# Kernel optimization log

Measured on AMD Instinct MI355X. Metric: run time of the kernel, lower is better.

The kernel has to match this reference:

```python
import jax, jax.numpy as jnp
import numpy as np

N = 50000        # num_nodes
E = 500000       # num_edges (avg degree 16)
EMB = 32         # node embedding dim
EDGE_DIM = 385   # EMBEDDING_DIM(384) + 1 grade
OC = 16          # out_channels
NEG_SLOPE = 0.2


def _gatv2(x, src, dst, eattr, Wl, bl, Wr, br, We, att, bias, heads, out_ch, n, concat):
    # lin_l -> source (x_j), lin_r -> target (x_i); PyG edge_index[0]=src, [1]=dst
    xl = (x @ Wl + bl).reshape(-1, heads, out_ch)   # [N,H,C]
    xr = (x @ Wr + br).reshape(-1, heads, out_ch)   # [N,H,C]
    ea = (eattr @ We).reshape(-1, heads, out_ch)    # [E,H,C]
    xj = xl[src]                                    # [E,H,C] gathered source
    xi = xr[dst]                                    # [E,H,C] gathered target
    e = jax.nn.leaky_relu(xj + xi + ea, NEG_SLOPE)
    logits = jnp.einsum('ehc,hc->eh', e, att)       # [E,H]
    # segment softmax over edges sharing the same target node
    m = jax.ops.segment_max(logits, dst, num_segments=n)
    m = jnp.where(jnp.isfinite(m), m, 0.0)
    ex = jnp.exp(logits - m[dst])
    s = jax.ops.segment_sum(ex, dst, num_segments=n)
    alpha = ex / (s[dst] + 1e-16)                   # [E,H]
    out = jax.ops.segment_sum(xj * alpha[..., None], dst, num_segments=n)  # [N,H,C]
    if concat:
        out = out.reshape(n, heads * out_ch)
    else:
        out = out.mean(axis=1)
    return out + bias


def setup_inputs() -> dict:
    key = jax.random.key(0)
    ks = jax.random.split(key, 32)
    f = lambda k, s, sc=0.1: (jax.random.normal(k, s, dtype=jnp.float32) * sc)
    inp = {}
    inp['node_ids'] = jnp.arange(N, dtype=jnp.int32)
    inp['edge_index'] = jax.random.randint(ks[0], (2, E), 0, N, dtype=jnp.int32)
    inp['edge_attr'] = f(ks[1], (E, EDGE_DIM))
    inp['node_emb'] = f(ks[2], (N, EMB))
    # layer 1: in=32, heads=4, out=16, concat -> 64
    inp['l1_Wl'] = f(ks[3], (EMB, 4 * OC)); inp['l1_bl'] = jnp.zeros((4 * OC,), jnp.float32)
    inp['l1_Wr'] = f(ks[4], (EMB, 4 * OC)); inp['l1_br'] = jnp.zeros((4 * OC,), jnp.float32)
    inp['l1_We'] = f(ks[5], (EDGE_DIM, 4 * OC))
    inp['l1_att'] = f(ks[6], (4, OC)); inp['l1_bias'] = jnp.zeros((4 * OC,), jnp.float32)
    # layer 2: in=64, heads=2, out=16, concat -> 32
    inp['l2_Wl'] = f(ks[7], (4 * OC, 2 * OC)); inp['l2_bl'] = jnp.zeros((2 * OC,), jnp.float32)
    inp['l2_Wr'] = f(ks[8], (4 * OC, 2 * OC)); inp['l2_br'] = jnp.zeros((2 * OC,), jnp.float32)
    inp['l2_We'] = f(ks[9], (EDGE_DIM, 2 * OC))
    inp['l2_att'] = f(ks[10], (2, OC)); inp['l2_bias'] = jnp.zeros((2 * OC,), jnp.float32)
    # layer 3: in=32, heads=1, out=16, mean -> 16
    inp['l3_Wl'] = f(ks[11], (2 * OC, OC)); inp['l3_bl'] = jnp.zeros((OC,), jnp.float32)
    inp['l3_Wr'] = f(ks[12], (2 * OC, OC)); inp['l3_br'] = jnp.zeros((OC,), jnp.float32)
    inp['l3_We'] = f(ks[13], (EDGE_DIM, OC))
    inp['l3_att'] = f(ks[14], (1, OC)); inp['l3_bias'] = jnp.zeros((OC,), jnp.float32)
    # edge MLP: 2*16 -> 64 -> 32 -> 1
    inp['mlp_W1'] = f(ks[15], (2 * OC, 64)); inp['mlp_b1'] = jnp.zeros((64,), jnp.float32)
    inp['mlp_W2'] = f(ks[16], (64, 32)); inp['mlp_b2'] = jnp.zeros((32,), jnp.float32)
    inp['mlp_W3'] = f(ks[17], (32, 1)); inp['mlp_b3'] = jnp.zeros((1,), jnp.float32)
    return inp


def reference(node_ids, edge_index, edge_attr, node_emb,
              l1_Wl, l1_bl, l1_Wr, l1_br, l1_We, l1_att, l1_bias,
              l2_Wl, l2_bl, l2_Wr, l2_br, l2_We, l2_att, l2_bias,
              l3_Wl, l3_bl, l3_Wr, l3_br, l3_We, l3_att, l3_bias,
              mlp_W1, mlp_b1, mlp_W2, mlp_b2, mlp_W3, mlp_b3):
    src, dst = edge_index[0], edge_index[1]
    x = node_emb[node_ids]                                   # [N,32]
    x1 = jax.nn.elu(_gatv2(x, src, dst, edge_attr, l1_Wl, l1_bl, l1_Wr, l1_br,
                           l1_We, l1_att, l1_bias, 4, OC, N, True))
    x2 = jax.nn.elu(_gatv2(x1, src, dst, edge_attr, l2_Wl, l2_bl, l2_Wr, l2_br,
                           l2_We, l2_att, l2_bias, 2, OC, N, True))
    x3 = _gatv2(x2, src, dst, edge_attr, l3_Wl, l3_bl, l3_Wr, l3_br,
                l3_We, l3_att, l3_bias, 1, OC, N, False)     # [N,16]
    h = jnp.concatenate([x3[src], x3[dst]], axis=1)          # [E,32]
    h = jax.nn.relu(h @ mlp_W1 + mlp_b1)
    h = jax.nn.relu(h @ mlp_W2 + mlp_b2)
    return (h @ mlp_W3 + mlp_b3).squeeze(-1)                 # [E]
```

## Files before the change

### kernel.cpp

```cpp
#include <hip/hip_runtime.h>

#define DEVINL __device__ __forceinline__

DEVINL unsigned fenc(float f) {
    unsigned u = __float_as_uint(f);
    return (u & 0x80000000u) ? ~u : (u | 0x80000000u);
}
DEVINL float fdec(unsigned k) {
    unsigned u = (k & 0x80000000u) ? (k ^ 0x80000000u) : ~k;
    return __uint_as_float(u);
}

DEVINL void gload_lds4(const float* g, float* l) {
    __builtin_amdgcn_global_load_lds(
        (const __attribute__((address_space(1))) unsigned int*)(const void*)g,
        (__attribute__((address_space(3))) unsigned int*)(void*)l,
        4, 0, 0);
}

__global__ void zero_kernel(float* __restrict__ p, long n) {
    long i = (long)blockIdx.x * blockDim.x + threadIdx.x;
    long stride = (long)gridDim.x * blockDim.x;
    for (; i < n; i += stride) p[i] = 0.f;
}

template<int IN, int HC>
__global__ __launch_bounds__(256) void node_transform(
    const float* __restrict__ x, const int* __restrict__ gather,
    const float* __restrict__ Wl, const float* __restrict__ bl,
    const float* __restrict__ Wr, const float* __restrict__ br,
    float* __restrict__ xl, float* __restrict__ xr, int N)
{
    __shared__ float Wls[IN * HC];
    __shared__ float Wrs[IN * HC];
    for (int i = threadIdx.x; i < IN * HC; i += 256) { Wls[i] = Wl[i]; Wrs[i] = Wr[i]; }
    __syncthreads();
    constexpr int NPB = 256 / HC;
    const int c = threadIdx.x % HC;
    const int n = blockIdx.x * NPB + threadIdx.x / HC;
    if (n >= N) return;
    const int row = gather ? gather[n] : n;
    const float* xp = x + (long)row * IN;
    float al = bl[c], ar = br[c];
#pragma unroll
    for (int k = 0; k < IN; ++k) {
        float v = xp[k];
        al = fmaf(v, Wls[k * HC + c], al);
        ar = fmaf(v, Wrs[k * HC + c], ar);
    }
    xl[(long)n * HC + c] = al;
    xr[(long)n * HC + c] = ar;
}

template<int HC, int OPT, int EPT>
__global__ __launch_bounds__(256) void gat_edge(
    const float* __restrict__ eattr,
    const float* __restrict__ xl, const float* __restrict__ xr,
    const float* __restrict__ We, const float* __restrict__ att,
    const int* __restrict__ src, const int* __restrict__ dst,
    float* __restrict__ logits, unsigned* __restrict__ mkey, int E)
{
    constexpr int H = HC / 16;
    constexpr int TX = HC / OPT;
    constexpr int TY = 256 / TX;
    constexpr int TILE_E = TY * EPT;
    constexpr int KC = 32;
    constexpr int NKM = 12;
    static_assert(TILE_E == 128, "tile geometry");
    static_assert((KC * HC) % 256 == 0, "B staging");
    static_assert((TILE_E * KC) / 256 == 16, "A staging");

    __shared__ float As[TILE_E * KC];
    __shared__ float Bs[KC * HC];
    __shared__ float Blast[HC];
    __shared__ float part[TILE_E][TX + 1];

    const int tid = threadIdx.x;
    const int tx = tid % TX, ty = tid / TX;
    const long eblk = (long)blockIdx.x * TILE_E;

    if (tid < HC) Blast[tid] = We[384 * HC + tid];

    float acc[EPT][OPT];
#pragma unroll
    for (int i = 0; i < EPT; ++i)
#pragma unroll
        for (int j = 0; j < OPT; ++j) acc[i][j] = 0.f;

    for (int kc = 0; kc < NKM; ++kc) {
        const int k0 = kc * KC;
#pragma unroll
        for (int i = 0; i < 16; ++i) {
            const int idx = tid + i * 256;
            const int row = idx >> 5;
            const int c   = idx & 31;
            const int klog = (((c >> 2) ^ ((row >> 2) & 7)) << 2) | (c & 3);
            long ge = eblk + row;
            ge = (ge < E) ? ge : (long)(E - 1);
            gload_lds4(eattr + ge * 385 + (k0 + klog), &As[idx]);
        }
        constexpr int BELEM = KC * HC / 256;
#pragma unroll
        for (int i = 0; i < BELEM; ++i) {
            const int idx = tid + i * 256;
            gload_lds4(We + (long)k0 * HC + idx, &Bs[idx]);
        }
        asm volatile("s_waitcnt vmcnt(0)" ::: "memory");
        __syncthreads();

#pragma unroll
        for (int g = 0; g < 8; ++g) {
            float a[EPT][4];
#pragma unroll
            for (int i = 0; i < EPT; ++i) {
                const int row = ty * EPT + i;
                const float4 v = *(const float4*)&As[row * KC + ((g ^ ((row >> 2) & 7)) << 2)];
                a[i][0] = v.x; a[i][1] = v.y; a[i][2] = v.z; a[i][3] = v.w;
            }
#pragma unroll
            for (int q = 0; q < 4; ++q) {
                float b[OPT];
#pragma unroll
                for (int j = 0; j < OPT; j += 4) {
                    const float4 bv = *(const float4*)&Bs[(g * 4 + q) * HC + tx * OPT + j];
                    b[j] = bv.x; b[j + 1] = bv.y; b[j + 2] = bv.z; b[j + 3] = bv.w;
                }
#pragma unroll
                for (int i = 0; i < EPT; ++i)
#pragma unroll
                    for (int j = 0; j < OPT; ++j)
                        acc[i][j] = fmaf(a[i][q], b[j], acc[i][j]);
            }
        }
        __syncthreads();
    }

    const int h = (tx * OPT) / 16;
    const int cb = (tx * OPT) % 16;
    float av[OPT], bl[OPT];
#pragma unroll
    for (int j = 0; j < OPT; ++j) {
        av[j] = att[h * 16 + cb + j];
        bl[j] = Blast[tx * OPT + j];
    }

#pragma unroll
    for (int i = 0; i < EPT; ++i) {
        const int el = ty * EPT + i;
        const long ge = eblk + el;
        float p = 0.f;
        if (ge < E) {
            const float a384 = eattr[ge * 385 + 384];
            const float* xlp = xl + (long)src[ge] * HC + tx * OPT;
            const float* xrp = xr + (long)dst[ge] * HC + tx * OPT;
#pragma unroll
            for (int j = 0; j < OPT; j += 4) {
                const float4 vj = *(const float4*)(xlp + j);
                const float4 vi = *(const float4*)(xrp + j);
                float t0 = fmaf(a384, bl[j + 0], acc[i][j + 0]) + vj.x + vi.x;
                float t1 = fmaf(a384, bl[j + 1], acc[i][j + 1]) + vj.y + vi.y;
                float t2 = fmaf(a384, bl[j + 2], acc[i][j + 2]) + vj.z + vi.z;
                float t3 = fmaf(a384, bl[j + 3], acc[i][j + 3]) + vj.w + vi.w;
                t0 = (t0 > 0.f) ? t0 : 0.2f * t0;
                t1 = (t1 > 0.f) ? t1 : 0.2f * t1;
                t2 = (t2 > 0.f) ? t2 : 0.2f * t2;
                t3 = (t3 > 0.f) ? t3 : 0.2f * t3;
                p = fmaf(t0, av[j + 0], p);
                p = fmaf(t1, av[j + 1], p);
                p = fmaf(t2, av[j + 2], p);
                p = fmaf(t3, av[j + 3], p);
            }
        }
        part[el][tx] = p;
    }
    __syncthreads();

    constexpr int G = 16 / OPT;
    for (int idx = tid; idx < TILE_E * H; idx += 256) {
        const int e = idx / H, hh = idx % H;
        const long ge = eblk + e;
        if (ge < E) {
            float l = 0.f;
#pragma unroll
            for (int g = 0; g < G; ++g) l += part[e][hh * G + g];
            logits[ge * H + hh] = l;
            atomicMax(&mkey[(unsigned)dst[ge] * H + hh], fenc(l));
        }
    }
}

template<int H>
__global__ __launch_bounds__(256) void softmax_ex(
    float* __restrict__ lg, const unsigned* __restrict__ mkey,
    float* __restrict__ ssum, const int* __restrict__ dst, int E)
{
    int idx = blockIdx.x * 256 + threadIdx.x;
    if (idx >= E * H) return;
    int e = idx / H, h = idx % H;
    int d = dst[e];
    float m = fdec(mkey[d * H + h]);
    float ex = expf(lg[idx] - m);
    lg[idx] = ex;
    atomicAdd(&ssum[d * H + h], ex);
}

template<int HC>
__global__ __launch_bounds__(256) void aggregate(
    const float* __restrict__ ex, const float* __restrict__ ssum,
    const float* __restrict__ xl, const int* __restrict__ src,
    const int* __restrict__ dst, float* __restrict__ acc, int E)
{
    constexpr int H = HC / 16;
    long idx = (long)blockIdx.x * 256 + threadIdx.x;
    if (idx >= (long)E * HC) return;
    int e = (int)(idx / HC), c = (int)(idx % HC);
    int h = c / 16;
    int d = dst[e];
    float alpha = ex[(long)e * H + h] / (ssum[d * H + h] + 1e-16f);
    atomicAdd(&acc[(long)d * HC + c], xl[(long)src[e] * HC + c] * alpha);
}

__global__ __launch_bounds__(256) void finalize_k(
    const float* __restrict__ acc, const float* __restrict__ bias,
    float* __restrict__ xout, int total, int HC, int do_elu)
{
    int idx = blockIdx.x * 256 + threadIdx.x;
    if (idx >= total) return;
    float v = acc[idx] + bias[idx % HC];
    if (do_elu) v = (v > 0.f) ? v : expm1f(v);
    xout[idx] = v;
}

__global__ __launch_bounds__(256) void edge_mlp(
    const float* __restrict__ x3, const int* __restrict__ src, const int* __restrict__ dst,
    const float* __restrict__ W1, const float* __restrict__ b1,
    const float* __restrict__ W2, const float* __restrict__ b2,
    const float* __restrict__ W3, const float* __restrict__ b3,
    float* __restrict__ out, int E)
{
    int e = blockIdx.x * 256 + threadIdx.x;
    if (e >= E) return;
    float in[32];
    const float* xs = x3 + (long)src[e] * 16;
    const float* xd = x3 + (long)dst[e] * 16;
#pragma unroll
    for (int k = 0; k < 16; k += 4) {
        float4 a = *(const float4*)(xs + k);
        float4 b = *(const float4*)(xd + k);
        in[k] = a.x; in[k + 1] = a.y; in[k + 2] = a.z; in[k + 3] = a.w;
        in[16 + k] = b.x; in[16 + k + 1] = b.y; in[16 + k + 2] = b.z; in[16 + k + 3] = b.w;
    }
    float h1[64];
#pragma unroll
    for (int j = 0; j < 64; ++j) h1[j] = b1[j];
#pragma unroll
    for (int k = 0; k < 32; ++k) {
        float a = in[k];
#pragma unroll
        for (int j = 0; j < 64; ++j) h1[j] = fmaf(a, W1[k * 64 + j], h1[j]);
    }
    float h2[32];
#pragma unroll
    for (int j = 0; j < 32; ++j) h2[j] = b2[j];
#pragma unroll
    for (int k = 0; k < 64; ++k) {
        float a = h1[k] > 0.f ? h1[k] : 0.f;
#pragma unroll
        for (int j = 0; j < 32; ++j) h2[j] = fmaf(a, W2[k * 32 + j], h2[j]);
    }
    float o = b3[0];
#pragma unroll
    for (int j = 0; j < 32; ++j) {
        float a = h2[j] > 0.f ? h2[j] : 0.f;
        o = fmaf(a, W3[j], o);
    }
    out[e] = o;
}

extern "C" void kernel_launch(void* const* d_in, const int* in_sizes, int n_in,
                              void* d_out, int out_size, void* d_ws, size_t ws_size,
                              hipStream_t stream) {
    const int N = in_sizes[0];
    const int E = in_sizes[1] / 2;

    const int*   node_ids = (const int*)d_in[0];
    const int*   src      = (const int*)d_in[1];
    const int*   dst      = src + E;
    const float* eattr    = (const float*)d_in[2];
    const float* node_emb = (const float*)d_in[3];
    const float* l1_Wl = (const float*)d_in[4],  *l1_bl = (const float*)d_in[5];
    const float* l1_Wr = (const float*)d_in[6],  *l1_br = (const float*)d_in[7];
    const float* l1_We = (const float*)d_in[8],  *l1_att = (const float*)d_in[9];
    const float* l1_bias = (const float*)d_in[10];
    const float* l2_Wl = (const float*)d_in[11], *l2_bl = (const float*)d_in[12];
    const float* l2_Wr = (const float*)d_in[13], *l2_br = (const float*)d_in[14];
    const float* l2_We = (const float*)d_in[15], *l2_att = (const float*)d_in[16];
    const float* l2_bias = (const float*)d_in[17];
    const float* l3_Wl = (const float*)d_in[18], *l3_bl = (const float*)d_in[19];
    const float* l3_Wr = (const float*)d_in[20], *l3_br = (const float*)d_in[21];
    const float* l3_We = (const float*)d_in[22], *l3_att = (const float*)d_in[23];
    const float* l3_bias = (const float*)d_in[24];
    const float* mW1 = (const float*)d_in[25], *mb1 = (const float*)d_in[26];
    const float* mW2 = (const float*)d_in[27], *mb2 = (const float*)d_in[28];
    const float* mW3 = (const float*)d_in[29], *mb3 = (const float*)d_in[30];
    float* out = (float*)d_out;

    float* base = (float*)d_ws;
    size_t o = 0;
    auto alloc = [&](size_t n) { float* p = base + o; o += (n + 63) & ~(size_t)63; return p; };
    float* acc1  = alloc((size_t)N * 64);
    float* acc2  = alloc((size_t)N * 32);
    float* acc3  = alloc((size_t)N * 16);
    float* ssum1 = alloc((size_t)N * 4);
    float* ssum2 = alloc((size_t)N * 2);
    float* ssum3 = alloc((size_t)N);
    unsigned* mkey1 = (unsigned*)alloc((size_t)N * 4);
    unsigned* mkey2 = (unsigned*)alloc((size_t)N * 2);
    unsigned* mkey3 = (unsigned*)alloc((size_t)N);
    const size_t zero_end = o;
    float* xl = alloc((size_t)N * 64);
    float* xr = alloc((size_t)N * 64);
    float* x1 = alloc((size_t)N * 64);
    float* x2 = alloc((size_t)N * 32);
    float* x3 = alloc((size_t)N * 16);
    float* lg1 = alloc((size_t)E * 4);
    float* lg2 = alloc((size_t)E * 2);
    float* lg3 = alloc((size_t)E);
    (void)ws_size; (void)n_in; (void)out_size;

    const int gridE2 = (E + 127) / 128;

    zero_kernel<<<1024, 256, 0, stream>>>(base, (long)zero_end);

    node_transform<32, 64><<<(N + 3) / 4, 256, 0, stream>>>(
        node_emb, node_ids, l1_Wl, l1_bl, l1_Wr, l1_br, xl, xr, N);
    gat_edge<64, 8, 4><<<gridE2, 256, 0, stream>>>(
        eattr, xl, xr, l1_We, l1_att, src, dst, lg1, mkey1, E);
    softmax_ex<4><<<(E * 4 + 255) / 256, 256, 0, stream>>>(lg1, mkey1, ssum1, dst, E);
    aggregate<64><<<(int)(((long)E * 64 + 255) / 256), 256, 0, stream>>>(
        lg1, ssum1, xl, src, dst, acc1, E);
    finalize_k<<<(N * 64 + 255) / 256, 256, 0, stream>>>(acc1, l1_bias, x1, N * 64, 64, 1);

    node_transform<64, 32><<<(N + 7) / 8, 256, 0, stream>>>(
        x1, nullptr, l2_Wl, l2_bl, l2_Wr, l2_br, xl, xr, N);
    gat_edge<32, 4, 4><<<gridE2, 256, 0, stream>>>(
        eattr, xl, xr, l2_We, l2_att, src, dst, lg2, mkey2, E);
    softmax_ex<2><<<(E * 2 + 255) / 256, 256, 0, stream>>>(lg2, mkey2, ssum2, dst, E);
    aggregate<32><<<(int)(((long)E * 32 + 255) / 256), 256, 0, stream>>>(
        lg2, ssum2, xl, src, dst, acc2, E);
    finalize_k<<<(N * 32 + 255) / 256, 256, 0, stream>>>(acc2, l2_bias, x2, N * 32, 32, 1);

    node_transform<32, 16><<<(N + 15) / 16, 256, 0, stream>>>(
        x2, nullptr, l3_Wl, l3_bl, l3_Wr, l3_br, xl, xr, N);
    gat_edge<16, 4, 2><<<gridE2, 256, 0, stream>>>(
        eattr, xl, xr, l3_We, l3_att, src, dst, lg3, mkey3, E);
    softmax_ex<1><<<(E + 255) / 256, 256, 0, stream>>>(lg3, mkey3, ssum3, dst, E);
    aggregate<16><<<(int)(((long)E * 16 + 255) / 256), 256, 0, stream>>>(
        lg3, ssum3, xl, src, dst, acc3, E);
    finalize_k<<<(N * 16 + 255) / 256, 256, 0, stream>>>(acc3, l3_bias, x3, N * 16, 16, 0);

    edge_mlp<<<(E + 255) / 256, 256, 0, stream>>>(
        x3, src, dst, mW1, mb1, mW2, mb2, mW3, mb3, out, E);
}
```

Before: 2.069 ms.

## Compute all three layers' edge-attribute projections in one pass over edge_attr

Packs the three We matrices into one 385x128 padded weight and runs a single double-buffered GEMM over edge_attr. It computes layer-1 logits and stores the layer-2 and layer-3 edge projections to small buffers, so the 770 MB edge_attr stream is read once instead of three times. Later layers use a lightweight logits kernel that reads those buffers, and the bias+ELU finalize for layers 1-2 is folded into the next node_transform. Aggregation now handles four channels per thread. The cost is extra writes of 48 floats per edge, 16 wasted padded columns in the GEMM, and higher register pressure from an 8x8 accumulator tile.

```diff
diff --git a/kernel.cpp b/kernel.cpp
--- a/kernel.cpp
+++ b/kernel.cpp
@@ -24,16 +24,33 @@
     for (; i < n; i += stride) p[i] = 0.f;
 }
 
-template<int IN, int HC>
+__global__ __launch_bounds__(256) void pack_w(
+    const float* __restrict__ We1, const float* __restrict__ We2,
+    const float* __restrict__ We3, float* __restrict__ Wp)
+{
+    int idx = blockIdx.x * 256 + threadIdx.x;
+    if (idx >= 385 * 128) return;
+    int k = idx >> 7, c = idx & 127;
+    float v = 0.f;
+    if (c < 64)       v = We1[k * 64 + c];
+    else if (c < 96)  v = We2[k * 32 + (c - 64)];
+    else if (c < 112) v = We3[k * 16 + (c - 96)];
+    Wp[idx] = v;
+}
+
+template<int IN, int HC, int PRE>
 __global__ __launch_bounds__(256) void node_transform(
     const float* __restrict__ x, const int* __restrict__ gather,
+    const float* __restrict__ pre_bias,
     const float* __restrict__ Wl, const float* __restrict__ bl,
     const float* __restrict__ Wr, const float* __restrict__ br,
     float* __restrict__ xl, float* __restrict__ xr, int N)
 {
     __shared__ float Wls[IN * HC];
     __shared__ float Wrs[IN * HC];
+    __shared__ float pbs[IN];
     for (int i = threadIdx.x; i < IN * HC; i += 256) { Wls[i] = Wl[i]; Wrs[i] = Wr[i]; }
+    if (PRE && threadIdx.x < IN) pbs[threadIdx.x] = pre_bias[threadIdx.x];
     __syncthreads();
     constexpr int NPB = 256 / HC;
     const int c = threadIdx.x % HC;
@@ -45,6 +62,7 @@
 #pragma unroll
     for (int k = 0; k < IN; ++k) {
         float v = xp[k];
+        if (PRE) { v += pbs[k]; v = (v > 0.f) ? v : expm1f(v); }
         al = fmaf(v, Wls[k * HC + c], al);
         ar = fmaf(v, Wrs[k * HC + c], ar);
     }
@@ -52,141 +70,218 @@
     xr[(long)n * HC + c] = ar;
 }
 
-template<int HC, int OPT, int EPT>
-__global__ __launch_bounds__(256) void gat_edge(
-    const float* __restrict__ eattr,
+__global__ __launch_bounds__(256) void ea_gat1(
+    const float* __restrict__ eattr, const float* __restrict__ Wpad,
     const float* __restrict__ xl, const float* __restrict__ xr,
-    const float* __restrict__ We, const float* __restrict__ att,
-    const int* __restrict__ src, const int* __restrict__ dst,
-    float* __restrict__ logits, unsigned* __restrict__ mkey, int E)
-{
-    constexpr int H = HC / 16;
-    constexpr int TX = HC / OPT;
-    constexpr int TY = 256 / TX;
-    constexpr int TILE_E = TY * EPT;
-    constexpr int KC = 32;
-    constexpr int NKM = 12;
-    static_assert(TILE_E == 128, "tile geometry");
-    static_assert((KC * HC) % 256 == 0, "B staging");
-    static_assert((TILE_E * KC) / 256 == 16, "A staging");
-
-    __shared__ float As[TILE_E * KC];
-    __shared__ float Bs[KC * HC];
-    __shared__ float Blast[HC];
-    __shared__ float part[TILE_E][TX + 1];
+    const float* __restrict__ att, const int* __restrict__ src,
+    const int* __restrict__ dst,
+    float* __restrict__ lg1, unsigned* __restrict__ mkey,
+    float* __restrict__ ea2, float* __restrict__ ea3, int E)
+{
+    constexpr int KC = 32, NKM = 12, COLS = 128, TILE_E = 128;
+    __shared__ float As[2][TILE_E * KC];
+    __shared__ float Bs[2][KC * COLS];
 
     const int tid = threadIdx.x;
-    const int tx = tid % TX, ty = tid / TX;
+    const int tx = tid & 15, ty = tid >> 4;
     const long eblk = (long)blockIdx.x * TILE_E;
 
-    if (tid < HC) Blast[tid] = We[384 * HC + tid];
-
-    float acc[EPT][OPT];
-#pragma unroll
-    for (int i = 0; i < EPT; ++i)
-#pragma unroll
-        for (int j = 0; j < OPT; ++j) acc[i][j] = 0.f;
-
-    for (int kc = 0; kc < NKM; ++kc) {
+    float acc[8][8];
+#pragma unroll
+    for (int i = 0; i < 8; ++i)
+#pragma unroll
+        for (int j = 0; j < 8; ++j) acc[i][j] = 0.f;
+
+    auto issue = [&](int buf, int kc) {
         const int k0 = kc * KC;
 #pragma unroll
         for (int i = 0; i < 16; ++i) {
             const int idx = tid + i * 256;
-            const int row = idx >> 5;
-            const int c   = idx & 31;
+            const int row = idx >> 5, c = idx & 31;
             const int klog = (((c >> 2) ^ ((row >> 2) & 7)) << 2) | (c & 3);
             long ge = eblk + row;
             ge = (ge < E) ? ge : (long)(E - 1);
-            gload_lds4(eattr + ge * 385 + (k0 + klog), &As[idx]);
-        }
-        constexpr int BELEM = KC * HC / 256;
-#pragma unroll
-        for (int i = 0; i < BELEM; ++i) {
+            gload_lds4(eattr + ge * 385 + (k0 + klog), &As[buf][idx]);
+        }
+#pragma unroll
+        for (int i = 0; i < 16; ++i) {
             const int idx = tid + i * 256;
-            gload_lds4(We + (long)k0 * HC + idx, &Bs[idx]);
-        }
-        asm volatile("s_waitcnt vmcnt(0)" ::: "memory");
-        __syncthreads();
-
+            gload_lds4(Wpad + (long)k0 * COLS + idx, &Bs[buf][idx]);
+        }
+    };
+
+    issue(0, 0);
+    int cur = 0;
+#pragma unroll 1
+    for (int kc = 0; kc < NKM; ++kc) {
+        if (kc + 1 < NKM) {
+            issue(cur ^ 1, kc + 1);
+            asm volatile("s_waitcnt vmcnt(32)" ::: "memory");
+        } else {
+            asm volatile("s_waitcnt vmcnt(0)" ::: "memory");
+        }
+        __builtin_amdgcn_s_barrier();
+        const float* Ab = As[cur];
+        const float* Bb = Bs[cur];
 #pragma unroll
         for (int g = 0; g < 8; ++g) {
-            float a[EPT][4];
-#pragma unroll
-            for (int i = 0; i < EPT; ++i) {
-                const int row = ty * EPT + i;
-                const float4 v = *(const float4*)&As[row * KC + ((g ^ ((row >> 2) & 7)) << 2)];
+            float a[8][4];
+#pragma unroll
+            for (int i = 0; i < 8; ++i) {
+                const int row = ty * 8 + i;
+                const float4 v = *(const float4*)&Ab[row * KC + ((g ^ ((row >> 2) & 7)) << 2)];
                 a[i][0] = v.x; a[i][1] = v.y; a[i][2] = v.z; a[i][3] = v.w;
             }
 #pragma unroll
             for (int q = 0; q < 4; ++q) {
-                float b[OPT];
-#pragma unroll
-                for (int j = 0; j < OPT; j += 4) {
-                    const float4 bv = *(const float4*)&Bs[(g * 4 + q) * HC + tx * OPT + j];
+                float b[8];
+#pragma unroll
+                for (int j = 0; j < 8; j += 4) {
+                    const float4 bv = *(const float4*)&Bb[(g * 4 + q) * COLS + tx * 8 + j];
                     b[j] = bv.x; b[j + 1] = bv.y; b[j + 2] = bv.z; b[j + 3] = bv.w;
                 }
 #pragma unroll
-                for (int i = 0; i < EPT; ++i)
-#pragma unroll
-                    for (int j = 0; j < OPT; ++j)
+                for (int i = 0; i < 8; ++i)
+#pragma unroll
+                    for (int j = 0; j < 8; ++j)
                         acc[i][j] = fmaf(a[i][q], b[j], acc[i][j]);
             }
         }
-        __syncthreads();
-    }
-
-    const int h = (tx * OPT) / 16;
-    const int cb = (tx * OPT) % 16;
-    float av[OPT], bl[OPT];
-#pragma unroll
-    for (int j = 0; j < OPT; ++j) {
-        av[j] = att[h * 16 + cb + j];
-        bl[j] = Blast[tx * OPT + j];
-    }
-
-#pragma unroll
-    for (int i = 0; i < EPT; ++i) {
-        const int el = ty * EPT + i;
-        const long ge = eblk + el;
-        float p = 0.f;
-        if (ge < E) {
-            const float a384 = eattr[ge * 385 + 384];
-            const float* xlp = xl + (long)src[ge] * HC + tx * OPT;
-            const float* xrp = xr + (long)dst[ge] * HC + tx * OPT;
-#pragma unroll
-            for (int j = 0; j < OPT; j += 4) {
-                const float4 vj = *(const float4*)(xlp + j);
-                const float4 vi = *(const float4*)(xrp + j);
-                float t0 = fmaf(a384, bl[j + 0], acc[i][j + 0]) + vj.x + vi.x;
-                float t1 = fmaf(a384, bl[j + 1], acc[i][j + 1]) + vj.y + vi.y;
-                float t2 = fmaf(a384, bl[j + 2], acc[i][j + 2]) + vj.z + vi.z;
-                float t3 = fmaf(a384, bl[j + 3], acc[i][j + 3]) + vj.w + vi.w;
-                t0 = (t0 > 0.f) ? t0 : 0.2f * t0;
-                t1 = (t1 > 0.f) ? t1 : 0.2f * t1;
-                t2 = (t2 > 0.f) ? t2 : 0.2f * t2;
-                t3 = (t3 > 0.f) ? t3 : 0.2f * t3;
-                p = fmaf(t0, av[j + 0], p);
-                p = fmaf(t1, av[j + 1], p);
-                p = fmaf(t2, av[j + 2], p);
-                p = fmaf(t3, av[j + 3], p);
+        __builtin_amdgcn_s_barrier();
+        cur ^= 1;
+    }
+
+    float (*part)[9] = reinterpret_cast<float(*)[9]>(&As[0][0]);
+
+    const int col0 = tx * 8;
+    float w384[8];
+#pragma unroll
+    for (int j = 0; j < 8; ++j) w384[j] = Wpad[384 * 128 + col0 + j];
+
+    if (col0 < 64) {
+        const int h = col0 >> 4, cb = col0 & 15;
+        float av[8];
+#pragma unroll
+        for (int j = 0; j < 8; ++j) av[j] = att[h * 16 + cb + j];
+#pragma unroll
+        for (int i = 0; i < 8; ++i) {
+            const int el = ty * 8 + i;
+            const long ge = eblk + el;
+            float p = 0.f;
+            if (ge < E) {
+                const float a384 = eattr[ge * 385 + 384];
+                const float* xlp = xl + (long)src[ge] * 64 + col0;
+                const float* xrp = xr + (long)dst[ge] * 64 + col0;
+#pragma unroll
+                for (int j = 0; j < 8; j += 4) {
+                    const float4 vj = *(const float4*)(xlp + j);
+                    const float4 vi = *(const float4*)(xrp + j);
+                    float t0 = fmaf(a384, w384[j + 0], acc[i][j + 0]) + vj.x + vi.x;
+                    float t1 = fmaf(a384, w384[j + 1], acc[i][j + 1]) + vj.y + vi.y;
+                    float t2 = fmaf(a384, w384[j + 2], acc[i][j + 2]) + vj.z + vi.z;
+                    float t3 = fmaf(a384, w384[j + 3], acc[i][j + 3]) + vj.w + vi.w;
+                    t0 = (t0 > 0.f) ? t0 : 0.2f * t0;
+                    t1 = (t1 > 0.f) ? t1 : 0.2f * t1;
+                    t2 = (t2 > 0.f) ? t2 : 0.2f * t2;
+                    t3 = (t3 > 0.f) ? t3 : 0.2f * t3;
+                    p = fmaf(t0, av[j + 0], p);
+                    p = fmaf(t1, av[j + 1], p);
+                    p = fmaf(t2, av[j + 2], p);
+                    p = fmaf(t3, av[j + 3], p);
+                }
             }
-        }
-        part[el][tx] = p;
+            part[el][tx] = p;
+        }
+    } else if (col0 < 96) {
+        const int c2 = col0 - 64;
+#pragma unroll
+        for (int i = 0; i < 8; ++i) {
+            const long ge = eblk + ty * 8 + i;
+            if (ge < E) {
+                const float a384 = eattr[ge * 385 + 384];
+                float4 o0, o1;
+                o0.x = fmaf(a384, w384[0], acc[i][0]);
+                o0.y = fmaf(a384, w384[1], acc[i][1]);
+                o0.z = fmaf(a384, w384[2], acc[i][2]);
+                o0.w = fmaf(a384, w384[3], acc[i][3]);
+                o1.x = fmaf(a384, w384[4], acc[i][4]);
+                o1.y = fmaf(a384, w384[5], acc[i][5]);
+                o1.z = fmaf(a384, w384[6], acc[i][6]);
+                o1.w = fmaf(a384, w384[7], acc[i][7]);
+                *(float4*)&ea2[ge * 32 + c2]     = o0;
+                *(float4*)&ea2[ge * 32 + c2 + 4] = o1;
+            }
+        }
+    } else if (col0 < 112) {
+        const int c3 = col0 - 96;
+#pragma unroll
+        for (int i = 0; i < 8; ++i) {
+            const long ge = eblk + ty * 8 + i;
+            if (ge < E) {
+                const float a384 = eattr[ge * 385 + 384];
+                float4 o0, o1;
+                o0.x = fmaf(a384, w384[0], acc[i][0]);
+                o0.y = fmaf(a384, w384[1], acc[i][1]);
+                o0.z = fmaf(a384, w384[2], acc[i][2]);
+                o0.w = fmaf(a384, w384[3], acc[i][3]);
+                o1.x = fmaf(a384, w384[4], acc[i][4]);
+                o1.y = fmaf(a384, w384[5], acc[i][5]);
+                o1.z = fmaf(a384, w384[6], acc[i][6]);
+                o1.w = fmaf(a384, w384[7], acc[i][7]);
+                *(float4*)&ea3[ge * 16 + c3]     = o0;
+                *(float4*)&ea3[ge * 16 + c3 + 4] = o1;
+            }
+        }
     }
     __syncthreads();
 
-    constexpr int G = 16 / OPT;
-    for (int idx = tid; idx < TILE_E * H; idx += 256) {
-        const int e = idx / H, hh = idx % H;
+    for (int idx = tid; idx < TILE_E * 4; idx += 256) {
+        const int e = idx >> 2, hh = idx & 3;
         const long ge = eblk + e;
         if (ge < E) {
-            float l = 0.f;
-#pragma unroll
-            for (int g = 0; g < G; ++g) l += part[e][hh * G + g];
-            logits[ge * H + hh] = l;
-            atomicMax(&mkey[(unsigned)dst[ge] * H + hh], fenc(l));
-        }
-    }
+            const float l = part[e][hh * 2] + part[e][hh * 2 + 1];
+            lg1[ge * 4 + hh] = l;
+            atomicMax(&mkey[(unsigned)dst[ge] * 4 + hh], fenc(l));
+        }
+    }
+}
+
+template<int H, int HC>
+__global__ __launch_bounds__(256) void edge_logits(
+    const float* __restrict__ ea, const float* __restrict__ xl,
+    const float* __restrict__ xr, const float* __restrict__ att,
+    const int* __restrict__ src, const int* __restrict__ dst,
+    float* __restrict__ lg, unsigned* __restrict__ mkey, int E)
+{
+    int idx = blockIdx.x * 256 + threadIdx.x;
+    if (idx >= E * H) return;
+    const int e = idx / H, h = idx % H;
+    const int s = src[e], d = dst[e];
+    const float* eap = ea + (long)e * HC + h * 16;
+    const float* xlp = xl + (long)s * HC + h * 16;
+    const float* xrp = xr + (long)d * HC + h * 16;
+    float p = 0.f;
+#pragma unroll
+    for (int j = 0; j < 16; j += 4) {
+        const float4 ev = *(const float4*)(eap + j);
+        const float4 vj = *(const float4*)(xlp + j);
+        const float4 vi = *(const float4*)(xrp + j);
+        const float4 av = *(const float4*)(att + h * 16 + j);
+        float t0 = ev.x + vj.x + vi.x;
+        float t1 = ev.y + vj.y + vi.y;
+        float t2 = ev.z + vj.z + vi.z;
+        float t3 = ev.w + vj.w + vi.w;
+        t0 = (t0 > 0.f) ? t0 : 0.2f * t0;
+        t1 = (t1 > 0.f) ? t1 : 0.2f * t1;
+        t2 = (t2 > 0.f) ? t2 : 0.2f * t2;
+        t3 = (t3 > 0.f) ? t3 : 0.2f * t3;
+        p = fmaf(t0, av.x, p);
+        p = fmaf(t1, av.y, p);
+        p = fmaf(t2, av.z, p);
+        p = fmaf(t3, av.w, p);
+    }
+    lg[idx] = p;
+    atomicMax(&mkey[(unsigned)d * H + h], fenc(p));
 }
 
 template<int H>
@@ -211,13 +306,19 @@
     const int* __restrict__ dst, float* __restrict__ acc, int E)
 {
     constexpr int H = HC / 16;
+    constexpr int C4 = HC / 4;
     long idx = (long)blockIdx.x * 256 + threadIdx.x;
-    if (idx >= (long)E * HC) return;
-    int e = (int)(idx / HC), c = (int)(idx % HC);
-    int h = c / 16;
-    int d = dst[e];
-    float alpha = ex[(long)e * H + h] / (ssum[d * H + h] + 1e-16f);
-    atomicAdd(&acc[(long)d * HC + c], xl[(long)src[e] * HC + c] * alpha);
+    if (idx >= (long)E * C4) return;
+    const int e = (int)(idx / C4), c4 = (int)(idx % C4);
+    const int c = c4 * 4, h = c >> 4;
+    const int d = dst[e], s = src[e];
+    const float alpha = ex[(long)e * H + h] / (ssum[d * H + h] + 1e-16f);
+    const float4 v = *(const float4*)&xl[(long)s * HC + c];
+    float* ap = &acc[(long)d * HC + c];
+    atomicAdd(ap + 0, v.x * alpha);
+    atomicAdd(ap + 1, v.y * alpha);
+    atomicAdd(ap + 2, v.z * alpha);
+    atomicAdd(ap + 3, v.w * alpha);
 }
 
 __global__ __launch_bounds__(256) void finalize_k(
@@ -318,44 +419,43 @@
     unsigned* mkey2 = (unsigned*)alloc((size_t)N * 2);
     unsigned* mkey3 = (unsigned*)alloc((size_t)N);
     const size_t zero_end = o;
-    float* xl = alloc((size_t)N * 64);
-    float* xr = alloc((size_t)N * 64);
-    float* x1 = alloc((size_t)N * 64);
-    float* x2 = alloc((size_t)N * 32);
-    float* x3 = alloc((size_t)N * 16);
+    float* xl  = alloc((size_t)N * 64);
+    float* xr  = alloc((size_t)N * 64);
+    float* x3  = alloc((size_t)N * 16);
+    float* ea2 = alloc((size_t)E * 32);
+    float* ea3 = alloc((size_t)E * 16);
     float* lg1 = alloc((size_t)E * 4);
     float* lg2 = alloc((size_t)E * 2);
     float* lg3 = alloc((size_t)E);
+    float* Wpad = alloc((size_t)385 * 128);
     (void)ws_size; (void)n_in; (void)out_size;
 
-    const int gridE2 = (E + 127) / 128;
-
     zero_kernel<<<1024, 256, 0, stream>>>(base, (long)zero_end);
-
-    node_transform<32, 64><<<(N + 3) / 4, 256, 0, stream>>>(
-        node_emb, node_ids, l1_Wl, l1_bl, l1_Wr, l1_br, xl, xr, N);
-    gat_edge<64, 8, 4><<<gridE2, 256, 0, stream>>>(
-        eattr, xl, xr, l1_We, l1_att, src, dst, lg1, mkey1, E);
+    pack_w<<<(385 * 128 + 255) / 256, 256, 0, stream>>>(l1_We, l2_We, l3_We, Wpad);
+
+    node_transform<32, 64, 0><<<(N + 3) / 4, 256, 0, stream>>>(
+        node_emb, node_ids, nullptr, l1_Wl, l1_bl, l1_Wr, l1_br, xl, xr, N);
+
+    ea_gat1<<<(E + 127) / 128, 256, 0, stream>>>(
+        eattr, Wpad, xl, xr, l1_att, src, dst, lg1, mkey1, ea2, ea3, E);
     softmax_ex<4><<<(E * 4 + 255) / 256, 256, 0, stream>>>(lg1, mkey1, ssum1, dst, E);
-    aggregate<64><<<(int)(((long)E * 64 + 255) / 256), 256, 0, stream>>>(
+    aggregate<64><<<(int)(((long)E * 16 + 255) / 256), 256, 0, stream>>>(
         lg1, ssum1, xl, src, dst, acc1, E);
-    finalize_k<<<(N * 64 + 255) / 256, 256, 0, stream>>>(acc1, l1_bias, x1, N * 64, 64, 1);
-
-    node_transform<64, 32><<<(N + 7) / 8, 256, 0, stream>>>(
-        x1, nullptr, l2_Wl, l2_bl, l2_Wr, l2_br, xl, xr, N);
-    gat_edge<32, 4, 4><<<gridE2, 256, 0, stream>>>(
-        eattr, xl, xr, l2_We, l2_att, src, dst, lg2, mkey2, E);
+
+    node_transform<64, 32, 1><<<(N + 7) / 8, 256, 0, stream>>>(
+        acc1, nullptr, l1_bias, l2_Wl, l2_bl, l2_Wr, l2_br, xl, xr, N);
+    edge_logits<2, 32><<<(E * 2 + 255) / 256, 256, 0, stream>>>(
+        ea2, xl, xr, l2_att, src, dst, lg2, mkey2, E);
     softmax_ex<2><<<(E * 2 + 255) / 256, 256, 0, stream>>>(lg2, mkey2, ssum2, dst, E);
-    aggregate<32><<<(int)(((long)E * 32 + 255) / 256), 256, 0, stream>>>(
+    aggregate<32><<<(int)(((long)E * 8 + 255) / 256), 256, 0, stream>>>(
         lg2, ssum2, xl, src, dst, acc2, E);
-    finalize_k<<<(N * 32 + 255) / 256, 256, 0, stream>>>(acc2, l2_bias, x2, N * 32, 32, 1);
-
-    node_transform<32, 16><<<(N + 15) / 16, 256, 0, stream>>>(
-        x2, nullptr, l3_Wl, l3_bl, l3_Wr, l3_br, xl, xr, N);
-    gat_edge<16, 4, 2><<<gridE2, 256, 0, stream>>>(
-        eattr, xl, xr, l3_We, l3_att, src, dst, lg3, mkey3, E);
+
+    node_transform<32, 16, 1><<<(N + 15) / 16, 256, 0, stream>>>(
+        acc2, nullptr, l2_bias, l3_Wl, l3_bl, l3_Wr, l3_br, xl, xr, N);
+    edge_logits<1, 16><<<(E + 255) / 256, 256, 0, stream>>>(
+        ea3, xl, xr, l3_att, src, dst, lg3, mkey3, E);
     softmax_ex<1><<<(E + 255) / 256, 256, 0, stream>>>(lg3, mkey3, ssum3, dst, E);
-    aggregate<16><<<(int)(((long)E * 16 + 255) / 256), 256, 0, stream>>>(
+    aggregate<16><<<(int)(((long)E * 4 + 255) / 256), 256, 0, stream>>>(
         lg3, ssum3, xl, src, dst, acc3, E);
     finalize_k<<<(N * 16 + 255) / 256, 256, 0, stream>>>(acc3, l3_bias, x3, N * 16, 16, 0);
 
```

Result: slower. 3.075 ms (+48.6%).
